# Kernel optimization log

Hardware: AMD Instinct MI355X
Metric: run time of the kernel (lower is better)

The kernel has to match this reference:

```python
import jax, jax.numpy as jnp
import numpy as np
from jax import lax

EPS = 1e-12  # F.normalize default eps


def setup_inputs() -> dict:
    key = jax.random.key(0)
    ks = jax.random.split(key, 4)
    b, dim, h, w = 8, 192, 128, 128
    num_heads = 6
    x = jax.random.normal(ks[0], (b, dim, h, w), dtype=jnp.float32)
    y = jax.random.normal(ks[1], (b, dim, h, w), dtype=jnp.float32)
    # depthwise conv weight (groups = 3*dim): [3*dim, 1, 3, 3]
    w_dw = jax.random.normal(ks[2], (3 * dim, 1, 3, 3), dtype=jnp.float32) * 0.1
    # 1x1 projection: [dim, dim]
    w_proj = jax.random.normal(ks[3], (dim, dim), dtype=jnp.float32) * (1.0 / np.sqrt(dim))
    temperature = jnp.ones((num_heads, 1, 1), dtype=jnp.float32)
    return {"x": x, "y": y, "w_dw": w_dw, "w_proj": w_proj,
            "temperature": temperature, "num_heads": num_heads}


def _l2norm(t):
    n = jnp.sqrt(jnp.sum(t * t, axis=-1, keepdims=True))
    return t / jnp.maximum(n, EPS)


def reference(x, y, w_dw, w_proj, temperature, num_heads):
    b, c, h, w = x.shape
    qkv_in = jnp.concatenate([x, y, y], axis=1)  # [b, 3c, h, w]
    # depthwise 3x3 conv, stride 1, padding 1 (groups = 3c)
    qkv = lax.conv_general_dilated(
        qkv_in, w_dw, window_strides=(1, 1), padding=((1, 1), (1, 1)),
        dimension_numbers=("NCHW", "OIHW", "NCHW"), feature_group_count=3 * c)
    q, k, v = jnp.split(qkv, 3, axis=1)
    ch = c // num_heads
    rs = lambda t: t.reshape(b, num_heads, ch, h * w)  # b head c (h w)
    q, k, v = rs(q), rs(k), rs(v)
    q = _l2norm(q)
    k = _l2norm(k)
    # channel attention: [b, head, ch, ch]
    attn = jnp.einsum("bhcn,bhdn->bhcd", q, k) * temperature
    attn = jax.nn.softmax(attn, axis=-1)
    out = jnp.einsum("bhcd,bhdn->bhcn", attn, v).reshape(b, c, h, w)
    # 1x1 conv projection
    out = jnp.einsum("oc,bchw->bohw", w_proj, out)
    return out
```

## Files before the change

kernel.cpp:

```cpp
#include <hip/hip_runtime.h>
#include <hip/hip_bf16.h>

#define DEV __device__ __forceinline__

typedef unsigned short u16;
typedef unsigned int u32;
typedef __attribute__((ext_vector_type(8))) short short8;
typedef __attribute__((ext_vector_type(4))) float f32x4;

DEV u16 f2bf(float f) {
  __hip_bfloat16 h = __float2bfloat16(f);
  return *(u16*)&h;
}
DEV float bf2f_s(short s) { return __uint_as_float(((u32)(u16)s) << 16); }

#define NB 8
#define NH 6
#define CTOT 192
#define HW 16384
#define QLD 136
#define VTS 34

DEV void loadrow10(float* d, const float* __restrict__ in, int ar, int c0) {
  const bool rok = (ar >= 0) && (ar < 128);
  const float* rp = in + ar * 128;
  d[0] = (rok && c0 > 0) ? rp[c0 - 1] : 0.0f;
  float4 f0, f1;
  if (rok) { f0 = *(const float4*)(rp + c0); f1 = *(const float4*)(rp + c0 + 4); }
  else { f0 = make_float4(0.f,0.f,0.f,0.f); f1 = f0; }
  d[1] = f0.x; d[2] = f0.y; d[3] = f0.z; d[4] = f0.w;
  d[5] = f1.x; d[6] = f1.y; d[7] = f1.z; d[8] = f1.w;
  d[9] = (rok && (c0 + 8) < 128) ? rp[c0 + 8] : 0.0f;
}

__global__ __launch_bounds__(256) void k1_fused(
    const float* __restrict__ x, const float* __restrict__ y,
    const float* __restrict__ wdw,
    u16* __restrict__ vt, float* __restrict__ gram,
    float* __restrict__ sqq, float* __restrict__ sqk)
{
  const int t   = threadIdx.x;
  const int bx  = blockIdx.x;
  const int chp = bx & 1;
  const int rg  = (bx >> 1) & 15;
  const int cg  = (bx >> 5) % 6;
  const int b   = bx / 192;
  const int cl  = t >> 3;
  const int colgrp = t & 7;
  const int gc  = cg * 32 + cl;
  const int c0  = chp * 64 + colgrp * 8;
  const int r0  = rg * 8;
  const int bh  = b * NH + cg;
  const int l    = t & 63, w = t >> 6;
  const int arow = l & 15;
  const int koff = w * 32 + ((l >> 4) << 3);

  __shared__ __align__(16) u16 q_lds[32 * QLD];
  __shared__ __align__(16) u16 k_lds[32 * QLD];
  __shared__ __align__(16) u16 vt_lds[2 * 64 * VTS];
  __shared__ __align__(16) float gram_lds[1024];

  *(f32x4*)&gram_lds[t * 4] = (f32x4){0.f, 0.f, 0.f, 0.f};

  const float* __restrict__ xin = x + (((size_t)(b * CTOT + gc)) << 14);
  const float* __restrict__ yin = y + (((size_t)(b * CTOT + gc)) << 14);

  float wq[9], wk[9], wv[9];
#pragma unroll
  for (int i = 0; i < 9; ++i) {
    wq[i] = wdw[gc * 9 + i];
    wk[i] = wdw[(CTOT + gc) * 9 + i];
    wv[i] = wdw[(2 * CTOT + gc) * 9 + i];
  }

  float xb[4][10], yb[4][10];
  loadrow10(xb[0], xin, r0 - 1, c0);
  loadrow10(yb[0], yin, r0 - 1, c0);
  loadrow10(xb[1], xin, r0,     c0);
  loadrow10(yb[1], yin, r0,     c0);
  loadrow10(xb[2], xin, r0 + 1, c0);
  loadrow10(yb[2], yin, r0 + 1, c0);

  f32x4 acc[2][2] = {};
  float sq[2] = {0.f, 0.f}, sk[2] = {0.f, 0.f};

#pragma unroll
  for (int ph = 0; ph < 4; ++ph) {
#pragma unroll
    for (int sub = 0; sub < 2; ++sub) {
      const int rr = ph * 2 + sub;
      const int r  = r0 + rr;
      if (rr < 7) {
        loadrow10(xb[(rr + 3) & 3], xin, r + 2, c0);
        loadrow10(yb[(rr + 3) & 3], yin, r + 2, c0);
      }

      float aq[8], ak[8], av[8];
#pragma unroll
      for (int j = 0; j < 8; ++j) { aq[j] = 0.f; ak[j] = 0.f; av[j] = 0.f; }
#pragma unroll
      for (int dr = 0; dr < 3; ++dr) {
#pragma unroll
        for (int j = 0; j < 8; ++j)
#pragma unroll
          for (int dc = 0; dc < 3; ++dc) {
            aq[j] = fmaf(wq[dr * 3 + dc], xb[(rr + dr) & 3][j + dc], aq[j]);
            ak[j] = fmaf(wk[dr * 3 + dc], yb[(rr + dr) & 3][j + dc], ak[j]);
            av[j] = fmaf(wv[dr * 3 + dc], yb[(rr + dr) & 3][j + dc], av[j]);
          }
      }
      short8 pq, pk;
#pragma unroll
      for (int j = 0; j < 8; ++j) {
        pq[j] = (short)f2bf(aq[j]);
        pk[j] = (short)f2bf(ak[j]);
      }
      *(short8*)&q_lds[cl * QLD + sub * 64 + colgrp * 8] = pq;
      *(short8*)&k_lds[cl * QLD + sub * 64 + colgrp * 8] = pk;
#pragma unroll
      for (int j = 0; j < 8; ++j)
        vt_lds[sub * 64 * VTS + (colgrp * 8 + j) * VTS + cl] = f2bf(av[j]);
    }
    __syncthreads();

    short8 a2[2], b2[2];
#pragma unroll
    for (int tc = 0; tc < 2; ++tc) {
      a2[tc] = *(const short8*)&q_lds[(tc * 16 + arow) * QLD + koff];
      b2[tc] = *(const short8*)&k_lds[(tc * 16 + arow) * QLD + koff];
    }
#pragma unroll
    for (int tc = 0; tc < 2; ++tc)
#pragma unroll
      for (int j = 0; j < 8; ++j) {
        float fa = bf2f_s(a2[tc][j]); sq[tc] = fmaf(fa, fa, sq[tc]);
        float fb = bf2f_s(b2[tc][j]); sk[tc] = fmaf(fb, fb, sk[tc]);
      }
#pragma unroll
    for (int tc = 0; tc < 2; ++tc)
#pragma unroll
      for (int td = 0; td < 2; ++td)
        acc[tc][td] = __builtin_amdgcn_mfma_f32_16x16x32_bf16(a2[tc], b2[td], acc[tc][td], 0, 0, 0);

    {
      const int sub  = t >> 7;
      const int col  = (t >> 1) & 63;
      const int half = (t & 1) * 16;
      const int r    = r0 + ph * 2 + sub;
      const int base = sub * 64 * VTS + col * VTS + half;
      short8 d0, d1;
#pragma unroll
      for (int j = 0; j < 8; ++j) { d0[j] = (short)vt_lds[base + j]; d1[j] = (short)vt_lds[base + 8 + j]; }
      size_t off = ((size_t)(b * HW + r * 128 + chp * 64 + col)) * CTOT + cg * 32 + half;
      *(short8*)(vt + off)     = d0;
      *(short8*)(vt + off + 8) = d1;
    }
    __syncthreads();
  }

#pragma unroll
  for (int tc = 0; tc < 2; ++tc)
#pragma unroll
    for (int td = 0; td < 2; ++td)
#pragma unroll
      for (int r2 = 0; r2 < 4; ++r2) {
        int c = tc * 16 + (l >> 4) * 4 + r2;
        int d = td * 16 + arow;
        atomicAdd(&gram_lds[c * 32 + d], acc[tc][td][r2]);
      }
  __syncthreads();
#pragma unroll
  for (int i = 0; i < 4; ++i)
    atomicAdd(gram + (size_t)bh * 1024 + t * 4 + i, gram_lds[t * 4 + i]);

#pragma unroll
  for (int tc = 0; tc < 2; ++tc) {
    sq[tc] += __shfl_xor(sq[tc], 16);
    sq[tc] += __shfl_xor(sq[tc], 32);
    sk[tc] += __shfl_xor(sk[tc], 16);
    sk[tc] += __shfl_xor(sk[tc], 32);
  }
  if ((l >> 4) == 0) {
#pragma unroll
    for (int tc = 0; tc < 2; ++tc) {
      atomicAdd(sqq + bh * 32 + tc * 16 + arow, sq[tc]);
      atomicAdd(sqk + bh * 32 + tc * 16 + arow, sk[tc]);
    }
  }
}

__global__ __launch_bounds__(256) void k2b_w2(
    const float* __restrict__ gram, const float* __restrict__ sqq,
    const float* __restrict__ sqk, const float* __restrict__ wp,
    const float* __restrict__ temp, u16* __restrict__ W2)
{
  __shared__ float Ls[32][33];
  __shared__ float As[32][33];
  __shared__ float wl[192 * 32];
  __shared__ float nq[32], nk[32];
  const int t = threadIdx.x;
  const int bh = blockIdx.x, b = bh / 6, h = bh % 6;
  const float tmp = temp[h];
  if (t < 32) nq[t] = fmaxf(sqrtf(sqq[bh * 32 + t]), 1e-12f);
  else if (t < 64) nk[t - 32] = fmaxf(sqrtf(sqk[bh * 32 + t - 32]), 1e-12f);
  __syncthreads();
#pragma unroll
  for (int i = 0; i < 4; ++i) {
    int idx = i * 256 + t, c = idx >> 5, d = idx & 31;
    Ls[c][d] = gram[(size_t)bh * 1024 + idx] / (nq[c] * nk[d]) * tmp;
  }
  __syncthreads();
  if (t < 32) {
    float m = -1e30f;
#pragma unroll
    for (int d = 0; d < 32; ++d) m = fmaxf(m, Ls[t][d]);
    float s = 0.f;
#pragma unroll
    for (int d = 0; d < 32; ++d) s += expf(Ls[t][d] - m);
    float inv = 1.0f / s;
#pragma unroll
    for (int d = 0; d < 32; ++d) As[t][d] = expf(Ls[t][d] - m) * inv;
  }
  for (int i = 0; i < 24; ++i) {
    int idx = i * 256 + t, o = idx >> 5, c = idx & 31;
    wl[idx] = wp[o * 192 + h * 32 + c];
  }
  __syncthreads();
  for (int i = 0; i < 24; ++i) {
    int idx = i * 256 + t, o = idx >> 5, d = idx & 31;
    float a = 0.f;
#pragma unroll
    for (int c = 0; c < 32; ++c) a = fmaf(wl[o * 32 + c], As[c][d], a);
    W2[((size_t)(b * 192 + o)) * 192 + h * 32 + d] = f2bf(a);
  }
}

__global__ __launch_bounds__(256) void k3_gemm(
    const u16* __restrict__ W2, const u16* __restrict__ vt,
    float* __restrict__ out)
{
  const int t = threadIdx.x, l = t & 63, w = t >> 6;
  const int bx = blockIdx.x;
  const int b  = bx >> 7, nb = bx & 127;
  const int row = l & 15;
  const int kq  = (l >> 4) * 8;
  const u16* w2b = W2 + (size_t)b * 192 * 192;
  const u16* vtb = vt + ((size_t)b << 14) * 192;
  const int n0 = nb * 128 + w * 32;

  f32x4 acc[12][2] = {};

  for (int ks = 0; ks < 6; ++ks) {
    const int kb = ks * 32 + kq;
    short8 bf[2];
#pragma unroll
    for (int nt = 0; nt < 2; ++nt)
      bf[nt] = *(const short8*)(vtb + (size_t)(n0 + nt * 16 + row) * 192 + kb);
#pragma unroll
    for (int ot = 0; ot < 12; ++ot) {
      short8 af = *(const short8*)(w2b + (size_t)(ot * 16 + row) * 192 + kb);
#pragma unroll
      for (int nt = 0; nt < 2; ++nt)
        acc[ot][nt] = __builtin_amdgcn_mfma_f32_16x16x32_bf16(af, bf[nt], acc[ot][nt], 0, 0, 0);
    }
  }

  float* ob = out + ((size_t)b * 192) * 16384;
#pragma unroll
  for (int ot = 0; ot < 12; ++ot)
#pragma unroll
    for (int nt = 0; nt < 2; ++nt)
#pragma unroll
      for (int rr = 0; rr < 4; ++rr) {
        int o = ot * 16 + (l >> 4) * 4 + rr;
        int n = n0 + nt * 16 + row;
        ob[(size_t)o * 16384 + n] = acc[ot][nt][rr];
      }
}

extern "C" void kernel_launch(void* const* d_in, const int* in_sizes, int n_in,
                              void* d_out, int out_size, void* d_ws, size_t ws_size,
                              hipStream_t stream)
{
  const float* x    = (const float*)d_in[0];
  const float* y    = (const float*)d_in[1];
  const float* wdw  = (const float*)d_in[2];
  const float* wp   = (const float*)d_in[3];
  const float* temp = (const float*)d_in[4];

  char* ws = (char*)d_ws;
  const size_t VT = (size_t)NB * HW * CTOT * 2;
  u16*   vt   = (u16*)(ws);
  float* gram = (float*)(ws + VT);
  float* sqq  = (float*)(ws + VT + 196608);
  float* sqk  = (float*)(ws + VT + 196608 + 6144);
  u16*   W2   = (u16*)(ws + VT + 196608 + 12288);
  float* out  = (float*)d_out;

  hipMemsetAsync(ws + VT, 0, 208896, stream);
  k1_fused<<<1536, 256, 0, stream>>>(x, y, wdw, vt, gram, sqq, sqk);
  k2b_w2<<<48, 256, 0, stream>>>(gram, sqq, sqk, wp, temp, W2);
  k3_gemm<<<1024, 256, 0, stream>>>(W2, vt, out);
}
```

Baseline: 180.2 us.

## Tile V transposed buffer in MFMA-fragment order and halve k1 column tile

The first kernel now covers 32 columns per block instead of 64, doubling the grid, and each thread computes 4 columns with a 3-row rolling buffer and lower register pressure. V is written to a new blocked layout that matches the MFMA B-fragment order, so the GEMM kernel reads contiguous 512-element chunks rather than rows strided by 192. The Gram MFMA work now runs on only two of the four waves, and the smaller tile brings more halo overhead and more global atomics per head.

```diff
diff --git a/kernel.cpp b/kernel.cpp
--- a/kernel.cpp
+++ b/kernel.cpp
@@ -18,19 +18,19 @@
 #define NH 6
 #define CTOT 192
 #define HW 16384
-#define QLD 136
-#define VTS 34
-
-DEV void loadrow10(float* d, const float* __restrict__ in, int ar, int c0) {
+#define QL2 72
+#define VTS2 40
+#define VT2_PER_B 3145728
+
+DEV void loadrow6(float* d, const float* __restrict__ in, int ar, int c0) {
   const bool rok = (ar >= 0) && (ar < 128);
   const float* rp = in + ar * 128;
   d[0] = (rok && c0 > 0) ? rp[c0 - 1] : 0.0f;
-  float4 f0, f1;
-  if (rok) { f0 = *(const float4*)(rp + c0); f1 = *(const float4*)(rp + c0 + 4); }
-  else { f0 = make_float4(0.f,0.f,0.f,0.f); f1 = f0; }
+  float4 f0;
+  if (rok) f0 = *(const float4*)(rp + c0);
+  else     f0 = make_float4(0.f, 0.f, 0.f, 0.f);
   d[1] = f0.x; d[2] = f0.y; d[3] = f0.z; d[4] = f0.w;
-  d[5] = f1.x; d[6] = f1.y; d[7] = f1.z; d[8] = f1.w;
-  d[9] = (rok && (c0 + 8) < 128) ? rp[c0 + 8] : 0.0f;
+  d[5] = (rok && (c0 + 4) < 128) ? rp[c0 + 4] : 0.0f;
 }
 
 __global__ __launch_bounds__(256) void k1_fused(
@@ -41,23 +41,23 @@
 {
   const int t   = threadIdx.x;
   const int bx  = blockIdx.x;
-  const int chp = bx & 1;
-  const int rg  = (bx >> 1) & 15;
-  const int cg  = (bx >> 5) % 6;
-  const int b   = bx / 192;
+  const int cp4 = bx & 3;
+  const int rg  = (bx >> 2) & 15;
+  const int cg  = (bx >> 6) % 6;
+  const int b   = bx / 384;
   const int cl  = t >> 3;
   const int colgrp = t & 7;
   const int gc  = cg * 32 + cl;
-  const int c0  = chp * 64 + colgrp * 8;
+  const int c0  = cp4 * 32 + colgrp * 4;
   const int r0  = rg * 8;
   const int bh  = b * NH + cg;
   const int l    = t & 63, w = t >> 6;
   const int arow = l & 15;
-  const int koff = w * 32 + ((l >> 4) << 3);
-
-  __shared__ __align__(16) u16 q_lds[32 * QLD];
-  __shared__ __align__(16) u16 k_lds[32 * QLD];
-  __shared__ __align__(16) u16 vt_lds[2 * 64 * VTS];
+  const int kq8  = (l >> 4) << 3;
+
+  __shared__ __align__(16) u16 q_lds[32 * QL2];
+  __shared__ __align__(16) u16 k_lds[32 * QL2];
+  __shared__ __align__(16) u16 vt_lds[2 * 32 * VTS2];
   __shared__ __align__(16) float gram_lds[1024];
 
   *(f32x4*)&gram_lds[t * 4] = (f32x4){0.f, 0.f, 0.f, 0.f};
@@ -73,16 +73,18 @@
     wv[i] = wdw[(2 * CTOT + gc) * 9 + i];
   }
 
-  float xb[4][10], yb[4][10];
-  loadrow10(xb[0], xin, r0 - 1, c0);
-  loadrow10(yb[0], yin, r0 - 1, c0);
-  loadrow10(xb[1], xin, r0,     c0);
-  loadrow10(yb[1], yin, r0,     c0);
-  loadrow10(xb[2], xin, r0 + 1, c0);
-  loadrow10(yb[2], yin, r0 + 1, c0);
+  float xb[3][6], yb[3][6];
+  loadrow6(xb[0], xin, r0 - 1, c0);
+  loadrow6(yb[0], yin, r0 - 1, c0);
+  loadrow6(xb[1], xin, r0,     c0);
+  loadrow6(yb[1], yin, r0,     c0);
 
   f32x4 acc[2][2] = {};
   float sq[2] = {0.f, 0.f}, sk[2] = {0.f, 0.f};
+
+  const int sub_s = t >> 7;
+  const int col_s = (t >> 2) & 31;
+  const int q_s   = t & 3;
 
 #pragma unroll
   for (int ph = 0; ph < 4; ++ph) {
@@ -90,101 +92,120 @@
     for (int sub = 0; sub < 2; ++sub) {
       const int rr = ph * 2 + sub;
       const int r  = r0 + rr;
-      if (rr < 7) {
-        loadrow10(xb[(rr + 3) & 3], xin, r + 2, c0);
-        loadrow10(yb[(rr + 3) & 3], yin, r + 2, c0);
-      }
-
-      float aq[8], ak[8], av[8];
-#pragma unroll
-      for (int j = 0; j < 8; ++j) { aq[j] = 0.f; ak[j] = 0.f; av[j] = 0.f; }
-#pragma unroll
-      for (int dr = 0; dr < 3; ++dr) {
-#pragma unroll
-        for (int j = 0; j < 8; ++j)
-#pragma unroll
-          for (int dc = 0; dc < 3; ++dc) {
-            aq[j] = fmaf(wq[dr * 3 + dc], xb[(rr + dr) & 3][j + dc], aq[j]);
-            ak[j] = fmaf(wk[dr * 3 + dc], yb[(rr + dr) & 3][j + dc], ak[j]);
-            av[j] = fmaf(wv[dr * 3 + dc], yb[(rr + dr) & 3][j + dc], av[j]);
-          }
-      }
-      short8 pq, pk;
-#pragma unroll
-      for (int j = 0; j < 8; ++j) {
-        pq[j] = (short)f2bf(aq[j]);
-        pk[j] = (short)f2bf(ak[j]);
-      }
-      *(short8*)&q_lds[cl * QLD + sub * 64 + colgrp * 8] = pq;
-      *(short8*)&k_lds[cl * QLD + sub * 64 + colgrp * 8] = pk;
-#pragma unroll
-      for (int j = 0; j < 8; ++j)
-        vt_lds[sub * 64 * VTS + (colgrp * 8 + j) * VTS + cl] = f2bf(av[j]);
+      loadrow6(xb[(rr + 2) % 3], xin, r + 1, c0);
+      loadrow6(yb[(rr + 2) % 3], yin, r + 1, c0);
+
+      {
+        float a[4];
+#pragma unroll
+        for (int j = 0; j < 4; ++j) a[j] = 0.f;
+#pragma unroll
+        for (int dr = 0; dr < 3; ++dr)
+#pragma unroll
+          for (int j = 0; j < 4; ++j)
+#pragma unroll
+            for (int dc = 0; dc < 3; ++dc)
+              a[j] = fmaf(wq[dr * 3 + dc], xb[(rr + dr) % 3][j + dc], a[j]);
+        u16* qp = &q_lds[cl * QL2 + sub * 32 + colgrp * 4];
+#pragma unroll
+        for (int j = 0; j < 4; ++j) qp[j] = f2bf(a[j]);
+      }
+      {
+        float a[4];
+#pragma unroll
+        for (int j = 0; j < 4; ++j) a[j] = 0.f;
+#pragma unroll
+        for (int dr = 0; dr < 3; ++dr)
+#pragma unroll
+          for (int j = 0; j < 4; ++j)
+#pragma unroll
+            for (int dc = 0; dc < 3; ++dc)
+              a[j] = fmaf(wk[dr * 3 + dc], yb[(rr + dr) % 3][j + dc], a[j]);
+        u16* kp = &k_lds[cl * QL2 + sub * 32 + colgrp * 4];
+#pragma unroll
+        for (int j = 0; j < 4; ++j) kp[j] = f2bf(a[j]);
+      }
+      {
+        float a[4];
+#pragma unroll
+        for (int j = 0; j < 4; ++j) a[j] = 0.f;
+#pragma unroll
+        for (int dr = 0; dr < 3; ++dr)
+#pragma unroll
+          for (int j = 0; j < 4; ++j)
+#pragma unroll
+            for (int dc = 0; dc < 3; ++dc)
+              a[j] = fmaf(wv[dr * 3 + dc], yb[(rr + dr) % 3][j + dc], a[j]);
+#pragma unroll
+        for (int j = 0; j < 4; ++j)
+          vt_lds[(sub * 32 + colgrp * 4 + j) * VTS2 + cl] = f2bf(a[j]);
+      }
     }
     __syncthreads();
 
-    short8 a2[2], b2[2];
-#pragma unroll
-    for (int tc = 0; tc < 2; ++tc) {
-      a2[tc] = *(const short8*)&q_lds[(tc * 16 + arow) * QLD + koff];
-      b2[tc] = *(const short8*)&k_lds[(tc * 16 + arow) * QLD + koff];
-    }
+    if (w < 2) {
+      short8 a2[2], b2[2];
+#pragma unroll
+      for (int tc = 0; tc < 2; ++tc) {
+        a2[tc] = *(const short8*)&q_lds[(tc * 16 + arow) * QL2 + w * 32 + kq8];
+        b2[tc] = *(const short8*)&k_lds[(tc * 16 + arow) * QL2 + w * 32 + kq8];
+      }
+#pragma unroll
+      for (int tc = 0; tc < 2; ++tc)
+#pragma unroll
+        for (int j = 0; j < 8; ++j) {
+          float fa = bf2f_s(a2[tc][j]); sq[tc] = fmaf(fa, fa, sq[tc]);
+          float fb = bf2f_s(b2[tc][j]); sk[tc] = fmaf(fb, fb, sk[tc]);
+        }
+#pragma unroll
+      for (int tc = 0; tc < 2; ++tc)
+#pragma unroll
+        for (int td = 0; td < 2; ++td)
+          acc[tc][td] = __builtin_amdgcn_mfma_f32_16x16x32_bf16(a2[tc], b2[td], acc[tc][td], 0, 0, 0);
+    }
+
+    {
+      const int r_s = r0 + ph * 2 + sub_s;
+      short8 d0 = *(short8*)&vt_lds[(sub_s * 32 + col_s) * VTS2 + q_s * 8];
+      size_t flat = (size_t)b * VT2_PER_B +
+          ((((((size_t)(r_s * 4 + cp4)) * 2 + (col_s >> 4)) * 6 + cg) * 16 + (col_s & 15)) * 32) +
+          q_s * 8;
+      *(short8*)(vt + flat) = d0;
+    }
+    __syncthreads();
+  }
+
+  if (w < 2) {
 #pragma unroll
     for (int tc = 0; tc < 2; ++tc)
 #pragma unroll
-      for (int j = 0; j < 8; ++j) {
-        float fa = bf2f_s(a2[tc][j]); sq[tc] = fmaf(fa, fa, sq[tc]);
-        float fb = bf2f_s(b2[tc][j]); sk[tc] = fmaf(fb, fb, sk[tc]);
-      }
-#pragma unroll
-    for (int tc = 0; tc < 2; ++tc)
-#pragma unroll
       for (int td = 0; td < 2; ++td)
-        acc[tc][td] = __builtin_amdgcn_mfma_f32_16x16x32_bf16(a2[tc], b2[td], acc[tc][td], 0, 0, 0);
-
-    {
-      const int sub  = t >> 7;
-      const int col  = (t >> 1) & 63;
-      const int half = (t & 1) * 16;
-      const int r    = r0 + ph * 2 + sub;
-      const int base = sub * 64 * VTS + col * VTS + half;
-      short8 d0, d1;
-#pragma unroll
-      for (int j = 0; j < 8; ++j) { d0[j] = (short)vt_lds[base + j]; d1[j] = (short)vt_lds[base + 8 + j]; }
-      size_t off = ((size_t)(b * HW + r * 128 + chp * 64 + col)) * CTOT + cg * 32 + half;
-      *(short8*)(vt + off)     = d0;
-      *(short8*)(vt + off + 8) = d1;
-    }
-    __syncthreads();
-  }
-
-#pragma unroll
-  for (int tc = 0; tc < 2; ++tc)
-#pragma unroll
-    for (int td = 0; td < 2; ++td)
-#pragma unroll
-      for (int r2 = 0; r2 < 4; ++r2) {
-        int c = tc * 16 + (l >> 4) * 4 + r2;
-        int d = td * 16 + arow;
-        atomicAdd(&gram_lds[c * 32 + d], acc[tc][td][r2]);
-      }
+#pragma unroll
+        for (int r2 = 0; r2 < 4; ++r2) {
+          int c = tc * 16 + (l >> 4) * 4 + r2;
+          int d = td * 16 + arow;
+          atomicAdd(&gram_lds[c * 32 + d], acc[tc][td][r2]);
+        }
+  }
   __syncthreads();
 #pragma unroll
   for (int i = 0; i < 4; ++i)
     atomicAdd(gram + (size_t)bh * 1024 + t * 4 + i, gram_lds[t * 4 + i]);
 
-#pragma unroll
-  for (int tc = 0; tc < 2; ++tc) {
-    sq[tc] += __shfl_xor(sq[tc], 16);
-    sq[tc] += __shfl_xor(sq[tc], 32);
-    sk[tc] += __shfl_xor(sk[tc], 16);
-    sk[tc] += __shfl_xor(sk[tc], 32);
-  }
-  if ((l >> 4) == 0) {
+  if (w < 2) {
 #pragma unroll
     for (int tc = 0; tc < 2; ++tc) {
-      atomicAdd(sqq + bh * 32 + tc * 16 + arow, sq[tc]);
-      atomicAdd(sqk + bh * 32 + tc * 16 + arow, sk[tc]);
+      sq[tc] += __shfl_xor(sq[tc], 16);
+      sq[tc] += __shfl_xor(sq[tc], 32);
+      sk[tc] += __shfl_xor(sk[tc], 16);
+      sk[tc] += __shfl_xor(sk[tc], 32);
+    }
+    if ((l >> 4) == 0) {
+#pragma unroll
+      for (int tc = 0; tc < 2; ++tc) {
+        atomicAdd(sqq + bh * 32 + tc * 16 + arow, sq[tc]);
+        atomicAdd(sqk + bh * 32 + tc * 16 + arow, sk[tc]);
+      }
     }
   }
 }
@@ -243,22 +264,22 @@
   const int bx = blockIdx.x;
   const int b  = bx >> 7, nb = bx & 127;
   const int row = l & 15;
-  const int kq  = (l >> 4) * 8;
+  const int kq8 = (l >> 4) * 8;
   const u16* w2b = W2 + (size_t)b * 192 * 192;
-  const u16* vtb = vt + ((size_t)b << 14) * 192;
+  const u16* vtb = vt + (size_t)b * VT2_PER_B;
   const int n0 = nb * 128 + w * 32;
 
   f32x4 acc[12][2] = {};
 
   for (int ks = 0; ks < 6; ++ks) {
-    const int kb = ks * 32 + kq;
     short8 bf[2];
 #pragma unroll
     for (int nt = 0; nt < 2; ++nt)
-      bf[nt] = *(const short8*)(vtb + (size_t)(n0 + nt * 16 + row) * 192 + kb);
+      bf[nt] = *(const short8*)(vtb +
+          ((size_t)(((nb * 4 + w) * 2 + nt) * 6 + ks)) * 512 + row * 32 + kq8);
 #pragma unroll
     for (int ot = 0; ot < 12; ++ot) {
-      short8 af = *(const short8*)(w2b + (size_t)(ot * 16 + row) * 192 + kb);
+      short8 af = *(const short8*)(w2b + (size_t)(ot * 16 + row) * 192 + ks * 32 + kq8);
 #pragma unroll
       for (int nt = 0; nt < 2; ++nt)
         acc[ot][nt] = __builtin_amdgcn_mfma_f32_16x16x32_bf16(af, bf[nt], acc[ot][nt], 0, 0, 0);
@@ -289,7 +310,7 @@
   const float* temp = (const float*)d_in[4];
 
   char* ws = (char*)d_ws;
-  const size_t VT = (size_t)NB * HW * CTOT * 2;
+  const size_t VT = (size_t)NB * VT2_PER_B * 2;
   u16*   vt   = (u16*)(ws);
   float* gram = (float*)(ws + VT);
   float* sqq  = (float*)(ws + VT + 196608);
@@ -298,7 +319,7 @@
   float* out  = (float*)d_out;
 
   hipMemsetAsync(ws + VT, 0, 208896, stream);
-  k1_fused<<<1536, 256, 0, stream>>>(x, y, wdw, vt, gram, sqq, sqk);
+  k1_fused<<<3072, 256, 0, stream>>>(x, y, wdw, vt, gram, sqq, sqk);
   k2b_w2<<<48, 256, 0, stream>>>(gram, sqq, sqk, wp, temp, W2);
   k3_gemm<<<1024, 256, 0, stream>>>(W2, vt, out);
 }
```

Result: slower. 212.1 us (+17.7%).

## Store V in native channel-major layout and transpose via LDS in projection GEMM

Applied to the files above, without the earlier changes.

The depthwise-conv kernel now writes V in its natural [b,c,hw] layout with direct vector stores instead of transposing through shared memory. It uses 4-row tiles (twice as many blocks) and computes q and k/v in separate passes with a single sync and one MFMA phase. The projection GEMM now loads V tiles into shared memory and transposes them there before the MFMAs. This moves the transpose cost from k1 to k3 and adds a shared-memory stage with barriers per k-step, while reducing k1 register pressure and sync count.

```diff
diff --git a/kernel.cpp b/kernel.cpp
--- a/kernel.cpp
+++ b/kernel.cpp
@@ -18,7 +18,7 @@
 #define NH 6
 #define CTOT 192
 #define HW 16384
-#define QLD 136
+#define QSTR 264
 #define VTS 34
 
 DEV void loadrow10(float* d, const float* __restrict__ in, int ar, int c0) {
@@ -36,28 +36,27 @@
 __global__ __launch_bounds__(256) void k1_fused(
     const float* __restrict__ x, const float* __restrict__ y,
     const float* __restrict__ wdw,
-    u16* __restrict__ vt, float* __restrict__ gram,
+    u16* __restrict__ vnat, float* __restrict__ gram,
     float* __restrict__ sqq, float* __restrict__ sqk)
 {
   const int t   = threadIdx.x;
   const int bx  = blockIdx.x;
   const int chp = bx & 1;
-  const int rg  = (bx >> 1) & 15;
-  const int cg  = (bx >> 5) % 6;
-  const int b   = bx / 192;
+  const int rg  = (bx >> 1) & 31;
+  const int cg  = (bx >> 6) % 6;
+  const int b   = bx / 384;
   const int cl  = t >> 3;
   const int colgrp = t & 7;
   const int gc  = cg * 32 + cl;
   const int c0  = chp * 64 + colgrp * 8;
-  const int r0  = rg * 8;
+  const int r0  = rg * 4;
   const int bh  = b * NH + cg;
   const int l    = t & 63, w = t >> 6;
   const int arow = l & 15;
-  const int koff = w * 32 + ((l >> 4) << 3);
-
-  __shared__ __align__(16) u16 q_lds[32 * QLD];
-  __shared__ __align__(16) u16 k_lds[32 * QLD];
-  __shared__ __align__(16) u16 vt_lds[2 * 64 * VTS];
+  const int kq8  = (l >> 4) << 3;
+
+  __shared__ __align__(16) u16 q_lds[32 * QSTR];
+  __shared__ __align__(16) u16 k_lds[32 * QSTR];
   __shared__ __align__(16) float gram_lds[1024];
 
   *(f32x4*)&gram_lds[t * 4] = (f32x4){0.f, 0.f, 0.f, 0.f};
@@ -65,98 +64,96 @@
   const float* __restrict__ xin = x + (((size_t)(b * CTOT + gc)) << 14);
   const float* __restrict__ yin = y + (((size_t)(b * CTOT + gc)) << 14);
 
-  float wq[9], wk[9], wv[9];
-#pragma unroll
-  for (int i = 0; i < 9; ++i) {
-    wq[i] = wdw[gc * 9 + i];
-    wk[i] = wdw[(CTOT + gc) * 9 + i];
-    wv[i] = wdw[(2 * CTOT + gc) * 9 + i];
-  }
-
-  float xb[4][10], yb[4][10];
-  loadrow10(xb[0], xin, r0 - 1, c0);
-  loadrow10(yb[0], yin, r0 - 1, c0);
-  loadrow10(xb[1], xin, r0,     c0);
-  loadrow10(yb[1], yin, r0,     c0);
-  loadrow10(xb[2], xin, r0 + 1, c0);
-  loadrow10(yb[2], yin, r0 + 1, c0);
+  {
+    float wq[9];
+#pragma unroll
+    for (int i = 0; i < 9; ++i) wq[i] = wdw[gc * 9 + i];
+    float rb[3][10];
+    loadrow10(rb[0], xin, r0 - 1, c0);
+    loadrow10(rb[1], xin, r0,     c0);
+#pragma unroll
+    for (int rl = 0; rl < 4; ++rl) {
+      loadrow10(rb[(rl + 2) % 3], xin, r0 + rl + 1, c0);
+      float a[8];
+#pragma unroll
+      for (int j = 0; j < 8; ++j) a[j] = 0.f;
+#pragma unroll
+      for (int dr = 0; dr < 3; ++dr)
+#pragma unroll
+        for (int j = 0; j < 8; ++j)
+#pragma unroll
+          for (int dc = 0; dc < 3; ++dc)
+            a[j] = fmaf(wq[dr * 3 + dc], rb[(rl + dr) % 3][j + dc], a[j]);
+      short8 p;
+#pragma unroll
+      for (int j = 0; j < 8; ++j) p[j] = (short)f2bf(a[j]);
+      *(short8*)&q_lds[cl * QSTR + rl * 64 + colgrp * 8] = p;
+    }
+  }
+
+  {
+    float wk[9], wv[9];
+#pragma unroll
+    for (int i = 0; i < 9; ++i) {
+      wk[i] = wdw[(CTOT + gc) * 9 + i];
+      wv[i] = wdw[(2 * CTOT + gc) * 9 + i];
+    }
+    float rb[3][10];
+    loadrow10(rb[0], yin, r0 - 1, c0);
+    loadrow10(rb[1], yin, r0,     c0);
+    u16* __restrict__ vout = vnat + (((size_t)(b * CTOT + gc)) << 14);
+#pragma unroll
+    for (int rl = 0; rl < 4; ++rl) {
+      loadrow10(rb[(rl + 2) % 3], yin, r0 + rl + 1, c0);
+      float ak[8], av[8];
+#pragma unroll
+      for (int j = 0; j < 8; ++j) { ak[j] = 0.f; av[j] = 0.f; }
+#pragma unroll
+      for (int dr = 0; dr < 3; ++dr)
+#pragma unroll
+        for (int j = 0; j < 8; ++j)
+#pragma unroll
+          for (int dc = 0; dc < 3; ++dc) {
+            ak[j] = fmaf(wk[dr * 3 + dc], rb[(rl + dr) % 3][j + dc], ak[j]);
+            av[j] = fmaf(wv[dr * 3 + dc], rb[(rl + dr) % 3][j + dc], av[j]);
+          }
+      short8 pk, pv;
+#pragma unroll
+      for (int j = 0; j < 8; ++j) { pk[j] = (short)f2bf(ak[j]); pv[j] = (short)f2bf(av[j]); }
+      *(short8*)&k_lds[cl * QSTR + rl * 64 + colgrp * 8] = pk;
+      *(short8*)(vout + (r0 + rl) * 128 + c0) = pv;
+    }
+  }
+
+  __syncthreads();
 
   f32x4 acc[2][2] = {};
-  float sq[2] = {0.f, 0.f}, sk[2] = {0.f, 0.f};
-
-#pragma unroll
-  for (int ph = 0; ph < 4; ++ph) {
-#pragma unroll
-    for (int sub = 0; sub < 2; ++sub) {
-      const int rr = ph * 2 + sub;
-      const int r  = r0 + rr;
-      if (rr < 7) {
-        loadrow10(xb[(rr + 3) & 3], xin, r + 2, c0);
-        loadrow10(yb[(rr + 3) & 3], yin, r + 2, c0);
+  float sq[2] = {0.f, 0.f}, sk2[2] = {0.f, 0.f};
+  short8 a2[2][2], b2[2][2];
+#pragma unroll
+  for (int tc = 0; tc < 2; ++tc)
+#pragma unroll
+    for (int kk = 0; kk < 2; ++kk) {
+      const int off = w * 64 + kk * 32 + kq8;
+      a2[tc][kk] = *(const short8*)&q_lds[(tc * 16 + arow) * QSTR + off];
+      b2[tc][kk] = *(const short8*)&k_lds[(tc * 16 + arow) * QSTR + off];
+    }
+#pragma unroll
+  for (int tc = 0; tc < 2; ++tc)
+#pragma unroll
+    for (int kk = 0; kk < 2; ++kk)
+#pragma unroll
+      for (int j = 0; j < 8; ++j) {
+        float fa = bf2f_s(a2[tc][kk][j]); sq[tc] = fmaf(fa, fa, sq[tc]);
+        float fb = bf2f_s(b2[tc][kk][j]); sk2[tc] = fmaf(fb, fb, sk2[tc]);
       }
-
-      float aq[8], ak[8], av[8];
-#pragma unroll
-      for (int j = 0; j < 8; ++j) { aq[j] = 0.f; ak[j] = 0.f; av[j] = 0.f; }
-#pragma unroll
-      for (int dr = 0; dr < 3; ++dr) {
-#pragma unroll
-        for (int j = 0; j < 8; ++j)
-#pragma unroll
-          for (int dc = 0; dc < 3; ++dc) {
-            aq[j] = fmaf(wq[dr * 3 + dc], xb[(rr + dr) & 3][j + dc], aq[j]);
-            ak[j] = fmaf(wk[dr * 3 + dc], yb[(rr + dr) & 3][j + dc], ak[j]);
-            av[j] = fmaf(wv[dr * 3 + dc], yb[(rr + dr) & 3][j + dc], av[j]);
-          }
-      }
-      short8 pq, pk;
-#pragma unroll
-      for (int j = 0; j < 8; ++j) {
-        pq[j] = (short)f2bf(aq[j]);
-        pk[j] = (short)f2bf(ak[j]);
-      }
-      *(short8*)&q_lds[cl * QLD + sub * 64 + colgrp * 8] = pq;
-      *(short8*)&k_lds[cl * QLD + sub * 64 + colgrp * 8] = pk;
-#pragma unroll
-      for (int j = 0; j < 8; ++j)
-        vt_lds[sub * 64 * VTS + (colgrp * 8 + j) * VTS + cl] = f2bf(av[j]);
-    }
-    __syncthreads();
-
-    short8 a2[2], b2[2];
-#pragma unroll
-    for (int tc = 0; tc < 2; ++tc) {
-      a2[tc] = *(const short8*)&q_lds[(tc * 16 + arow) * QLD + koff];
-      b2[tc] = *(const short8*)&k_lds[(tc * 16 + arow) * QLD + koff];
-    }
+#pragma unroll
+  for (int kk = 0; kk < 2; ++kk)
 #pragma unroll
     for (int tc = 0; tc < 2; ++tc)
 #pragma unroll
-      for (int j = 0; j < 8; ++j) {
-        float fa = bf2f_s(a2[tc][j]); sq[tc] = fmaf(fa, fa, sq[tc]);
-        float fb = bf2f_s(b2[tc][j]); sk[tc] = fmaf(fb, fb, sk[tc]);
-      }
-#pragma unroll
-    for (int tc = 0; tc < 2; ++tc)
-#pragma unroll
       for (int td = 0; td < 2; ++td)
-        acc[tc][td] = __builtin_amdgcn_mfma_f32_16x16x32_bf16(a2[tc], b2[td], acc[tc][td], 0, 0, 0);
-
-    {
-      const int sub  = t >> 7;
-      const int col  = (t >> 1) & 63;
-      const int half = (t & 1) * 16;
-      const int r    = r0 + ph * 2 + sub;
-      const int base = sub * 64 * VTS + col * VTS + half;
-      short8 d0, d1;
-#pragma unroll
-      for (int j = 0; j < 8; ++j) { d0[j] = (short)vt_lds[base + j]; d1[j] = (short)vt_lds[base + 8 + j]; }
-      size_t off = ((size_t)(b * HW + r * 128 + chp * 64 + col)) * CTOT + cg * 32 + half;
-      *(short8*)(vt + off)     = d0;
-      *(short8*)(vt + off + 8) = d1;
-    }
-    __syncthreads();
-  }
+        acc[tc][td] = __builtin_amdgcn_mfma_f32_16x16x32_bf16(a2[tc][kk], b2[td][kk], acc[tc][td], 0, 0, 0);
 
 #pragma unroll
   for (int tc = 0; tc < 2; ++tc)
@@ -175,16 +172,16 @@
 
 #pragma unroll
   for (int tc = 0; tc < 2; ++tc) {
-    sq[tc] += __shfl_xor(sq[tc], 16);
-    sq[tc] += __shfl_xor(sq[tc], 32);
-    sk[tc] += __shfl_xor(sk[tc], 16);
-    sk[tc] += __shfl_xor(sk[tc], 32);
+    sq[tc]  += __shfl_xor(sq[tc], 16);
+    sq[tc]  += __shfl_xor(sq[tc], 32);
+    sk2[tc] += __shfl_xor(sk2[tc], 16);
+    sk2[tc] += __shfl_xor(sk2[tc], 32);
   }
   if ((l >> 4) == 0) {
 #pragma unroll
     for (int tc = 0; tc < 2; ++tc) {
       atomicAdd(sqq + bh * 32 + tc * 16 + arow, sq[tc]);
-      atomicAdd(sqk + bh * 32 + tc * 16 + arow, sk[tc]);
+      atomicAdd(sqk + bh * 32 + tc * 16 + arow, sk2[tc]);
     }
   }
 }
@@ -236,29 +233,40 @@
 }
 
 __global__ __launch_bounds__(256) void k3_gemm(
-    const u16* __restrict__ W2, const u16* __restrict__ vt,
+    const u16* __restrict__ W2, const u16* __restrict__ vnat,
     float* __restrict__ out)
 {
+  __shared__ __align__(16) u16 b_tile[128 * VTS];
   const int t = threadIdx.x, l = t & 63, w = t >> 6;
   const int bx = blockIdx.x;
   const int b  = bx >> 7, nb = bx & 127;
-  const int row = l & 15;
-  const int kq  = (l >> 4) * 8;
+  const int arow = l & 15;
+  const int kq8  = (l >> 4) * 8;
   const u16* w2b = W2 + (size_t)b * 192 * 192;
-  const u16* vtb = vt + ((size_t)b << 14) * 192;
-  const int n0 = nb * 128 + w * 32;
+  const u16* vb  = vnat + ((size_t)b * CTOT) * HW;
+  const int n0 = nb * 128;
 
   f32x4 acc[12][2] = {};
 
   for (int ks = 0; ks < 6; ++ks) {
-    const int kb = ks * 32 + kq;
+    if (ks > 0) __syncthreads();
+#pragma unroll
+    for (int r2 = 0; r2 < 2; ++r2) {
+      const int ch   = (t >> 4) + r2 * 16;
+      const int nseg = (t & 15) * 8;
+      short8 vv = *(const short8*)(vb + (size_t)(ks * 32 + ch) * HW + n0 + nseg);
+#pragma unroll
+      for (int j = 0; j < 8; ++j) b_tile[(nseg + j) * VTS + ch] = (u16)vv[j];
+    }
+    __syncthreads();
+
     short8 bf[2];
 #pragma unroll
     for (int nt = 0; nt < 2; ++nt)
-      bf[nt] = *(const short8*)(vtb + (size_t)(n0 + nt * 16 + row) * 192 + kb);
+      bf[nt] = *(const short8*)&b_tile[(w * 32 + nt * 16 + arow) * VTS + kq8];
 #pragma unroll
     for (int ot = 0; ot < 12; ++ot) {
-      short8 af = *(const short8*)(w2b + (size_t)(ot * 16 + row) * 192 + kb);
+      short8 af = *(const short8*)(w2b + (size_t)(ot * 16 + arow) * 192 + ks * 32 + kq8);
 #pragma unroll
       for (int nt = 0; nt < 2; ++nt)
         acc[ot][nt] = __builtin_amdgcn_mfma_f32_16x16x32_bf16(af, bf[nt], acc[ot][nt], 0, 0, 0);
@@ -273,7 +281,7 @@
 #pragma unroll
       for (int rr = 0; rr < 4; ++rr) {
         int o = ot * 16 + (l >> 4) * 4 + rr;
-        int n = n0 + nt * 16 + row;
+        int n = n0 + w * 32 + nt * 16 + arow;
         ob[(size_t)o * 16384 + n] = acc[ot][nt][rr];
       }
 }
@@ -290,7 +298,7 @@
 
   char* ws = (char*)d_ws;
   const size_t VT = (size_t)NB * HW * CTOT * 2;
-  u16*   vt   = (u16*)(ws);
+  u16*   vnat = (u16*)(ws);
   float* gram = (float*)(ws + VT);
   float* sqq  = (float*)(ws + VT + 196608);
   float* sqk  = (float*)(ws + VT + 196608 + 6144);
@@ -298,7 +306,7 @@
   float* out  = (float*)d_out;
 
   hipMemsetAsync(ws + VT, 0, 208896, stream);
-  k1_fused<<<1536, 256, 0, stream>>>(x, y, wdw, vt, gram, sqq, sqk);
+  k1_fused<<<3072, 256, 0, stream>>>(x, y, wdw, vnat, gram, sqq, sqk);
   k2b_w2<<<48, 256, 0, stream>>>(gram, sqq, sqk, wp, temp, W2);
-  k3_gemm<<<1024, 256, 0, stream>>>(W2, vt, out);
-}
+  k3_gemm<<<1024, 256, 0, stream>>>(W2, vnat, out);
+}
```

Result: slower. 208.9 us (+15.9%).
